# Kernel tuning notes

Hardware: AMD Instinct MI355X
Metric: run time of the kernel (lower is better)

Reference implementation:

```python
import jax, jax.numpy as jnp
import numpy as np

N_BANKS = 16
BAND = 4
D = 32          # n_neurons_per_hidd_bank
N_IN = 3072     # n_input_neurons
N_OUT = 1000    # n_output_neurons
B = 8192        # batch size
IDX_INPUT = [0, 1]
IDX_OUTPUT = [14, 15]
# edge list (source, target), target-major, ascending sources per target --
# matches the torch loop order (np.where over bank_conn[:, i_target])
EDGES = [(s, t) for t in range(N_BANKS) for s in range(max(0, t - BAND), t)]
E = len(EDGES)  # 54
TGT_EDGES = [[e for e, (s, t) in enumerate(EDGES) if t == tt] for tt in range(N_BANKS)]
BN_EPS = 1e-5


def _bn(a):
    # BatchNorm1d in training mode: batch mean, biased batch variance
    m = a.mean(axis=0)
    v = a.var(axis=0)
    return (a - m) * jax.lax.rsqrt(v + BN_EPS)


def setup_inputs() -> dict:
    key = jax.random.key(0)
    ks = jax.random.split(key, 8)
    return {
        "x": jax.random.normal(ks[0], (B, N_IN), jnp.float32),
        "bn_gamma": jnp.ones((N_IN,), jnp.float32),
        "bn_beta": jnp.zeros((N_IN,), jnp.float32),
        "W_in": jax.random.normal(ks[1], (len(IDX_INPUT), N_IN, D), jnp.float32) / np.float32(np.sqrt(N_IN)),
        "b_in": jax.random.normal(ks[2], (len(IDX_INPUT), D), jnp.float32) / np.float32(np.sqrt(N_IN)),
        "Wg": jax.random.normal(ks[3], (E, D), jnp.float32) / np.float32(np.sqrt(D)),
        "Wd": jax.random.normal(ks[4], (E, D, D), jnp.float32) / np.float32(np.sqrt(D)),
        "bd": jax.random.normal(ks[5], (E, D), jnp.float32) / np.float32(np.sqrt(D)),
        "Wout": jax.random.normal(ks[6], (len(IDX_OUTPUT), D, N_OUT), jnp.float32) / np.float32(np.sqrt(D)),
    }


def reference(x, bn_gamma, bn_beta, W_in, b_in, Wg, Wd, bd, Wout):
    # input batch norm (affine)
    x = _bn(x) * bn_gamma + bn_beta
    acts = [None] * N_BANKS
    for k, i in enumerate(IDX_INPUT):
        acts[i] = jax.nn.relu(x @ W_in[k] + b_in[k])  # [B, D]
    total_gate = jnp.zeros((x.shape[0], 1), x.dtype)
    for t in range(N_BANKS):
        acc = acts[t]  # non-None only for input banks
        for e in TGT_EDGES[t]:
            s = EDGES[e][0]
            gate = jnp.clip(acts[s] @ Wg[e], 0.0, 1.0)[:, None]  # hardtanh(.,0,1), [B,1]
            total_gate = total_gate + gate
            data = acts[s] @ Wd[e] + bd[e]                       # [B, D]
            acc = gate * data if acc is None else acc + gate * data
        acts[t] = _bn(jax.nn.relu(acc))  # hidden batch norm, affine=False
    output = None
    for k, i in enumerate(IDX_OUTPUT):
        d = acts[i] @ Wout[k]  # Linear(D, N_OUT, bias=False)
        output = d if output is None else output + d
    return output, total_gate
```

## Files before the change

kernel.cpp:

```cpp
#include <hip/hip_runtime.h>


#define BATCH 8192
#define NIN 3072
#define DD 32
#define NB 16
#define NOUT 1000
#define TGOFF (BATCH * NOUT)
#define BNEPS 1e-5f
#define NBLK 256
#define ROWS 32

#define O_SUM 0
#define O_FLAG 0
#define O_SUM2 3072
#define O_STATS2 6144
#define O_TG 22528
#define ZERO_FLOATS 30720
#define O_SCALE 30720
#define O_SHIFT 33792
#define O_BIAS 36864
#define O_BP 36928
#define O_ACTS 233536
#define O_ACC (O_ACTS + 2 * BATCH * DD)

__global__ void __launch_bounds__(256) k_stats(const float* __restrict__ x, float* __restrict__ ws) {
    int c = blockIdx.x * 256 + threadIdx.x;
    const float* p = x + (size_t)blockIdx.y * 128 * NIN + c;
    float s = 0.f, s2 = 0.f;
#pragma unroll 8
    for (int i = 0; i < 128; i++) { float v = p[(size_t)i * NIN]; s += v; s2 += v * v; }
    atomicAdd(&ws[O_SUM + c], s);
    atomicAdd(&ws[O_SUM2 + c], s2);
}

__global__ void __launch_bounds__(256) k_prep(float* __restrict__ ws, const float* __restrict__ g,
                                              const float* __restrict__ b, const float* __restrict__ b_in) {
    int c = blockIdx.x * 256 + threadIdx.x;
    float mean = ws[O_SUM + c] * (1.f / BATCH);
    float var = ws[O_SUM2 + c] * (1.f / BATCH) - mean * mean;
    float sc = g[c] * rsqrtf(fmaxf(var, 0.f) + BNEPS);
    ws[O_SCALE + c] = sc;
    ws[O_SHIFT + c] = b[c] - mean * sc;
    if (c < 64) ws[O_BIAS + c] = b_in[c];
}

__global__ void __launch_bounds__(256) k_bias(float* __restrict__ ws, const float* __restrict__ W_in) {
    int bank = blockIdx.x & 1, jc = blockIdx.x >> 1;
    int d = threadIdx.x & 31, js = threadIdx.x >> 5;
    int j0 = jc * 256 + js * 32;
    float a = 0.f;
    for (int j = 0; j < 32; j++)
        a += ws[O_SHIFT + j0 + j] * W_in[(size_t)bank * NIN * DD + (size_t)(j0 + j) * DD + d];
    __shared__ float red[8][32];
    red[js][d] = a;
    __syncthreads();
    if (threadIdx.x < 32) {
        float t = 0.f;
#pragma unroll
        for (int g8 = 0; g8 < 8; g8++) t += red[g8][threadIdx.x];
        atomicAdd(&ws[O_BIAS + bank * 32 + threadIdx.x], t);
    }
}

__global__ void __launch_bounds__(256) k_bfold(float* __restrict__ ws, const float* __restrict__ W_in) {
    int idx = blockIdx.x * 256 + threadIdx.x;
    int j = idx >> 6, c = idx & 63;
    ws[O_BP + idx] = ws[O_SCALE + j] * W_in[(size_t)(c >> 5) * NIN * DD + (size_t)j * DD + (c & 31)];
}

__global__ void __launch_bounds__(256) k_gemm3(const float* __restrict__ x, float* __restrict__ ws) {
    __shared__ float xL[64][20];
    __shared__ float bL[16][64];
    int tid = threadIdx.x;
    int row0 = blockIdx.x * 64;
    int k00 = blockIdx.y * 768;
    const float* bp = ws + O_BP;
    float acc[4][4] = {};
    int tx = tid & 15, rt = tid >> 4;
    int lr = tid >> 2, lq = tid & 3;
    int br = tid >> 4, bq = tid & 15;
    for (int kc = 0; kc < 48; kc++) {
        int k0 = k00 + kc * 16;
        float4 xv = *(const float4*)&x[(size_t)(row0 + lr) * NIN + k0 + lq * 4];
        float4 bv = *(const float4*)&bp[(size_t)(k0 + br) * 64 + bq * 4];
        __syncthreads();
        *(float4*)&xL[lr][lq * 4] = xv;
        *(float4*)&bL[br][bq * 4] = bv;
        __syncthreads();
#pragma unroll
        for (int kk = 0; kk < 16; kk += 4) {
            float4 b0 = *(float4*)&bL[kk][tx * 4];
            float4 b1 = *(float4*)&bL[kk + 1][tx * 4];
            float4 b2 = *(float4*)&bL[kk + 2][tx * 4];
            float4 b3 = *(float4*)&bL[kk + 3][tx * 4];
#pragma unroll
            for (int j = 0; j < 4; j++) {
                float4 xv4 = *(float4*)&xL[rt * 4 + j][kk];
                acc[j][0] += xv4.x * b0.x + xv4.y * b1.x + xv4.z * b2.x + xv4.w * b3.x;
                acc[j][1] += xv4.x * b0.y + xv4.y * b1.y + xv4.z * b2.y + xv4.w * b3.y;
                acc[j][2] += xv4.x * b0.z + xv4.y * b1.z + xv4.z * b2.z + xv4.w * b3.z;
                acc[j][3] += xv4.x * b0.w + xv4.y * b1.w + xv4.z * b2.w + xv4.w * b3.w;
            }
        }
    }
    float* dst = ws + O_ACC + (size_t)blockIdx.y * (BATCH * 64);
#pragma unroll
    for (int j = 0; j < 4; j++) {
        float4 v = make_float4(acc[j][0], acc[j][1], acc[j][2], acc[j][3]);
        *(float4*)&dst[(size_t)(row0 + rt * 4 + j) * 64 + tx * 4] = v;
    }
}

__global__ void __launch_bounds__(256) k_act(float* __restrict__ ws) {
    __shared__ float sred[16][32];
    __shared__ float qred[16][32];
    int tid = threadIdx.x;
    int i4 = (blockIdx.x * 256 + tid) * 4;
    const float* ac = ws + O_ACC;
    float4 s0 = *(const float4*)&ac[i4];
    float4 s1 = *(const float4*)&ac[524288 + i4];
    float4 s2 = *(const float4*)&ac[1048576 + i4];
    float4 s3 = *(const float4*)&ac[1572864 + i4];
    int c = i4 & 63, row = i4 >> 6;
    const float* bias = ws + O_BIAS;
    float4 v;
    v.x = fmaxf(s0.x + s1.x + s2.x + s3.x + bias[c], 0.f);
    v.y = fmaxf(s0.y + s1.y + s2.y + s3.y + bias[c + 1], 0.f);
    v.z = fmaxf(s0.z + s1.z + s2.z + s3.z + bias[c + 2], 0.f);
    v.w = fmaxf(s0.w + s1.w + s2.w + s3.w + bias[c + 3], 0.f);
    int bank = c >> 5, dd = c & 31;
    *(float4*)&ws[O_ACTS + ((size_t)bank * BATCH + row) * DD + dd] = v;
    int r16 = tid >> 4;
    if (bank == 0) {
        *(float4*)&sred[r16][dd] = v;
        *(float4*)&qred[r16][dd] = make_float4(v.x * v.x, v.y * v.y, v.z * v.z, v.w * v.w);
    }
    __syncthreads();
    if (tid < 32) {
        float sm = 0.f, sq = 0.f;
#pragma unroll
        for (int r = 0; r < 16; r++) { sm += sred[r][tid]; sq += qred[r][tid]; }
        int slot = blockIdx.x & 3;
        float* st = ws + O_STATS2 + (size_t)slot * 64;
        atomicAdd(&st[tid], sm);
        atomicAdd(&st[32 + tid], sq);
    }
}

__global__ void __launch_bounds__(256, 2) k_banks(float* __restrict__ ws,
                                                  const float* __restrict__ Wg,
                                                  const float* __restrict__ Wd,
                                                  const float* __restrict__ bd) {
    __shared__ float ring[4][ROWS][32];
    __shared__ float WdL[2][4][1024];
    __shared__ float sred4[4][64];
    __shared__ float m_s[32], iv_s[32];
    __shared__ float red[8][64];
    int tid = threadIdx.x;
    int rg = tid >> 5, d = tid & 31;
    int row0 = blockIdx.x * ROWS;
    int slot4 = blockIdx.x & 3;
    float* acts = ws + O_ACTS;
    float* stats = ws + O_STATS2;
    int* flag = (int*)(ws + O_FLAG);
    float tg[4] = {0.f, 0.f, 0.f, 0.f};
    float cur[4];
#pragma unroll
    for (int ri = 0; ri < 4; ri++) {
        int r = rg + 8 * ri;
        ring[0][r][d] = acts[(size_t)(row0 + r) * DD + d];
        cur[ri] = acts[((size_t)BATCH + row0 + r) * DD + d];
    }
    sred4[tid >> 6][tid & 63] = stats[(size_t)(tid >> 6) * 64 + (tid & 63)];
    __syncthreads();
    if (tid < 32) {
        float sm = sred4[0][tid] + sred4[1][tid] + sred4[2][tid] + sred4[3][tid];
        float sq = sred4[0][32 + tid] + sred4[1][32 + tid] + sred4[2][32 + tid] + sred4[3][32 + tid];
        float m = sm * (1.f / BATCH);
        float var = sq * (1.f / BATCH) - m * m;
        m_s[tid] = m;
        iv_s[tid] = rsqrtf(fmaxf(var, 0.f) + BNEPS);
    }
    ((float4*)&WdL[1][0][0])[tid] = ((const float4*)Wd)[tid];
    __syncthreads();
#pragma unroll
    for (int ri = 0; ri < 4; ri++) {
        int r = rg + 8 * ri;
        ring[0][r][d] = (ring[0][r][d] - m_s[d]) * iv_s[d];
    }
    __syncthreads();
    for (int t = 1; t < 16; t++) {
        int buf = t & 1;
        int nE = t < 4 ? t : 4;
        int s0 = t - nE;
        int eb = (t <= 4) ? t * (t - 1) / 2 : 10 + 4 * (t - 5);
        if (t < 15) {
            int t2 = t + 1;
            int nE2 = t2 < 4 ? t2 : 4;
            int eb2 = (t2 <= 4) ? t2 * (t2 - 1) / 2 : 10 + 4 * (t2 - 5);
            for (int p = tid; p < nE2 * 256; p += 256)
                ((float4*)&WdL[buf ^ 1][0][0])[p] = ((const float4*)(Wd + (size_t)eb2 * 1024))[p];
        }
        float wgr[4], bdr[4];
#pragma unroll
        for (int ei = 0; ei < 4; ei++) {
            wgr[ei] = (ei < nE) ? Wg[(eb + ei) * 32 + d] : 0.f;
            bdr[ei] = (ei < nE) ? bd[(eb + ei) * 32 + d] : 0.f;
        }
        float c_[4];
#pragma unroll
        for (int ri = 0; ri < 4; ri++) c_[ri] = (t == 1) ? cur[ri] : 0.f;
#pragma unroll
        for (int ei = 0; ei < 3; ei++) {
            if (ei < nE - 1) {
                int sl = (s0 + ei) & 3;
#pragma unroll
                for (int ri = 0; ri < 4; ri++) {
                    int r = rg + 8 * ri;
                    float g = ring[sl][r][d] * wgr[ei];
                    g += __shfl_xor(g, 1); g += __shfl_xor(g, 2); g += __shfl_xor(g, 4);
                    g += __shfl_xor(g, 8); g += __shfl_xor(g, 16);
                    g = fminf(fmaxf(g, 0.f), 1.f);
                    tg[ri] += g;
                    float dat = bdr[ei];
                    const float* ar = ring[sl][r];
                    const float* wc = &WdL[buf][ei][d];
#pragma unroll
                    for (int k = 0; k < 32; k += 4) {
                        float4 a4 = *(const float4*)&ar[k];
                        dat += a4.x * wc[k * 32] + a4.y * wc[(k + 1) * 32]
                             + a4.z * wc[(k + 2) * 32] + a4.w * wc[(k + 3) * 32];
                    }
                    c_[ri] += g * dat;
                }
            }
        }
        if (t > 1) {
            if (tid == 0) {
                while (__hip_atomic_load(&flag[t - 1], __ATOMIC_RELAXED, __HIP_MEMORY_SCOPE_AGENT) < NBLK)
                    __builtin_amdgcn_s_sleep(8);
            }
            __syncthreads();
            sred4[tid >> 6][tid & 63] = __hip_atomic_load(
                &stats[((size_t)(t - 1) * 4 + (tid >> 6)) * 64 + (tid & 63)],
                __ATOMIC_RELAXED, __HIP_MEMORY_SCOPE_AGENT);
            __syncthreads();
            if (tid < 32) {
                float sm = sred4[0][tid] + sred4[1][tid] + sred4[2][tid] + sred4[3][tid];
                float sq = sred4[0][32 + tid] + sred4[1][32 + tid] + sred4[2][32 + tid] + sred4[3][32 + tid];
                float m = sm * (1.f / BATCH);
                float var = sq * (1.f / BATCH) - m * m;
                m_s[tid] = m;
                iv_s[tid] = rsqrtf(fmaxf(var, 0.f) + BNEPS);
            }
            __syncthreads();
            int sl = (t - 1) & 3;
#pragma unroll
            for (int ri = 0; ri < 4; ri++) {
                int r = rg + 8 * ri;
                ring[sl][r][d] = (ring[sl][r][d] - m_s[d]) * iv_s[d];
            }
            __syncthreads();
        }
        {
            int ei = nE - 1;
            int sl = (t - 1) & 3;
#pragma unroll
            for (int ri = 0; ri < 4; ri++) {
                int r = rg + 8 * ri;
                float g = ring[sl][r][d] * wgr[ei];
                g += __shfl_xor(g, 1); g += __shfl_xor(g, 2); g += __shfl_xor(g, 4);
                g += __shfl_xor(g, 8); g += __shfl_xor(g, 16);
                g = fminf(fmaxf(g, 0.f), 1.f);
                tg[ri] += g;
                float dat = bdr[ei];
                const float* ar = ring[sl][r];
                const float* wc = &WdL[buf][ei][d];
#pragma unroll
                for (int k = 0; k < 32; k += 4) {
                    float4 a4 = *(const float4*)&ar[k];
                    dat += a4.x * wc[k * 32] + a4.y * wc[(k + 1) * 32]
                         + a4.z * wc[(k + 2) * 32] + a4.w * wc[(k + 3) * 32];
                }
                c_[ri] += g * dat;
            }
        }
        float vv[4];
#pragma unroll
        for (int ri = 0; ri < 4; ri++) vv[ri] = fmaxf(c_[ri], 0.f);
        __syncthreads();
#pragma unroll
        for (int ri = 0; ri < 4; ri++) {
            int r = rg + 8 * ri;
            ring[t & 3][r][d] = vv[ri];
            if (t >= 14) acts[((size_t)t * BATCH + row0 + r) * DD + d] = vv[ri];
        }
        red[rg][d] = vv[0] + vv[1] + vv[2] + vv[3];
        red[rg][32 + d] = vv[0] * vv[0] + vv[1] * vv[1] + vv[2] * vv[2] + vv[3] * vv[3];
        __syncthreads();
        if (tid < 64) {
            float a = 0.f;
#pragma unroll
            for (int g8 = 0; g8 < 8; g8++) a += red[g8][tid];
            atomicAdd(&stats[((size_t)t * 4 + slot4) * 64 + tid], a);
        }
        if (t < 15) {
            __syncthreads();
            if (tid == 0) atomicAdd(&flag[t], 1);
        }
    }
    if (d == 0) {
#pragma unroll
        for (int ri = 0; ri < 4; ri++) ws[O_TG + row0 + rg + 8 * ri] = tg[ri];
    }
}

__global__ void __launch_bounds__(256) k_out(const float* __restrict__ ws, const float* __restrict__ Wout,
                                             float* __restrict__ out) {
    __shared__ float aLt[32][68];
    __shared__ float wL[32][128];
    __shared__ float mIv[2][2][32];
    int tid = threadIdx.x;
    int row0 = blockIdx.x * 64;
    int col0 = blockIdx.y * 128;
    const float* acts = ws + O_ACTS;
    if (blockIdx.y == 0 && tid < 64) out[TGOFF + row0 + tid] = ws[O_TG + row0 + tid];
    if (tid < 64) {
        int bi = tid >> 5, d = tid & 31;
        const float* st = ws + O_STATS2 + (size_t)(14 + bi) * 4 * 64;
        float sm = 0.f, sq = 0.f;
#pragma unroll
        for (int sl = 0; sl < 4; sl++) { sm += st[sl * 64 + d]; sq += st[sl * 64 + 32 + d]; }
        float m = sm * (1.f / BATCH);
        float var = sq * (1.f / BATCH) - m * m;
        mIv[bi][0][d] = m;
        mIv[bi][1][d] = rsqrtf(fmaxf(var, 0.f) + BNEPS);
    }
    int tx = tid & 31, ty = tid >> 5;
    int c4 = col0 + tx * 4;
    bool c4ok = (c4 + 3 < NOUT);
    float acc[8][4] = {};
    for (int bi = 0; bi < 2; bi++) {
        __syncthreads();
        {
            int d = tid & 31, r0 = tid >> 5;
            float m = mIv[bi][0][d], iv = mIv[bi][1][d];
            const float* ap = acts + ((size_t)(14 + bi) * BATCH + row0) * DD + d;
#pragma unroll
            for (int i = 0; i < 8; i++) {
                int r = r0 + 8 * i;
                aLt[d][r] = (ap[(size_t)r * DD] - m) * iv;
            }
        }
        {
            const float* wp = Wout + (size_t)bi * DD * NOUT + c4;
            int kk0 = tid >> 5;
#pragma unroll
            for (int i = 0; i < 4; i++) {
                int kk = kk0 + 8 * i;
                const float* wr = wp + (size_t)kk * NOUT;
                float4 v;
                if (c4ok) {
                    v = *(const float4*)wr;
                } else {
                    v.x = (c4 + 0 < NOUT) ? wr[0] : 0.f;
                    v.y = (c4 + 1 < NOUT) ? wr[1] : 0.f;
                    v.z = (c4 + 2 < NOUT) ? wr[2] : 0.f;
                    v.w = (c4 + 3 < NOUT) ? wr[3] : 0.f;
                }
                *(float4*)&wL[kk][tx * 4] = v;
            }
        }
        __syncthreads();
#pragma unroll 4
        for (int k = 0; k < 32; k++) {
            float4 w = *(float4*)&wL[k][tx * 4];
            float4 a0 = *(float4*)&aLt[k][ty * 8];
            float4 a1 = *(float4*)&aLt[k][ty * 8 + 4];
            float ar[8] = {a0.x, a0.y, a0.z, a0.w, a1.x, a1.y, a1.z, a1.w};
            float wc[4] = {w.x, w.y, w.z, w.w};
#pragma unroll
            for (int r = 0; r < 8; r++)
#pragma unroll
                for (int c = 0; c < 4; c++)
                    acc[r][c] += ar[r] * wc[c];
        }
    }
    if (c4ok) {
#pragma unroll
        for (int r = 0; r < 8; r++) {
            int row = row0 + ty * 8 + r;
            *(float4*)&out[(size_t)row * NOUT + c4] =
                make_float4(acc[r][0], acc[r][1], acc[r][2], acc[r][3]);
        }
    } else {
#pragma unroll
        for (int r = 0; r < 8; r++) {
            int row = row0 + ty * 8 + r;
#pragma unroll
            for (int c = 0; c < 4; c++)
                if (c4 + c < NOUT) out[(size_t)row * NOUT + c4 + c] = acc[r][c];
        }
    }
}

extern "C" void kernel_launch(void* const* d_in, const int* in_sizes, int n_in,
                              void* d_out, int out_size, void* d_ws, size_t ws_size,
                              hipStream_t stream) {
    (void)in_sizes; (void)n_in; (void)out_size; (void)ws_size;
    const float* x     = (const float*)d_in[0];
    const float* gamma = (const float*)d_in[1];
    const float* beta  = (const float*)d_in[2];
    const float* W_in  = (const float*)d_in[3];
    const float* b_in  = (const float*)d_in[4];
    const float* Wg    = (const float*)d_in[5];
    const float* Wd    = (const float*)d_in[6];
    const float* bd    = (const float*)d_in[7];
    const float* Wout  = (const float*)d_in[8];
    float* out = (float*)d_out;
    float* ws  = (float*)d_ws;

    hipMemsetAsync(d_ws, 0, ZERO_FLOATS * sizeof(float), stream);
    k_stats<<<dim3(12, 64), 256, 0, stream>>>(x, ws);
    k_prep<<<12, 256, 0, stream>>>(ws, gamma, beta, b_in);
    k_bias<<<24, 256, 0, stream>>>(ws, W_in);
    k_bfold<<<768, 256, 0, stream>>>(ws, W_in);
    k_gemm3<<<dim3(128, 4), 256, 0, stream>>>(x, ws);
    k_act<<<512, 256, 0, stream>>>(ws);
    hipMemsetAsync(ws + O_FLAG, 0, 16 * sizeof(int), stream);
    k_banks<<<NBLK, 256, 0, stream>>>(ws, Wg, Wd, bd);
    k_out<<<dim3(128, 8), 256, 0, stream>>>(ws, Wout, out);
}
```

Baseline: 375.8 us.

## Split input GEMM finer and spread bank-sync stats and flags over eight slots

The input-projection GEMM now uses 32-row tiles with 6-way split-K, launching 1536 blocks instead of 512 so more CUs stay busy. k_act sums six partial slices to match. In the bank pipeline, batch-norm statistics and completion flags are spread over 8 slots instead of 4 and a single counter, to cut atomic contention. Waiting blocks poll the eight flag counters with one wavefront and sleep for shorter intervals. The cost is more split-K partial traffic and a larger workspace for the partial sums.

```diff
diff --git a/kernel.cpp b/kernel.cpp
--- a/kernel.cpp
+++ b/kernel.cpp
@@ -10,6 +10,7 @@
 #define BNEPS 1e-5f
 #define NBLK 256
 #define ROWS 32
+#define NSLOT 8
 
 #define O_SUM 0
 #define O_FLAG 0
@@ -70,22 +71,22 @@
 }
 
 __global__ void __launch_bounds__(256) k_gemm3(const float* __restrict__ x, float* __restrict__ ws) {
-    __shared__ float xL[64][20];
+    __shared__ float xL[32][20];
     __shared__ float bL[16][64];
     int tid = threadIdx.x;
-    int row0 = blockIdx.x * 64;
-    int k00 = blockIdx.y * 768;
+    int row0 = blockIdx.x * 32;
+    int k00 = blockIdx.y * 512;
     const float* bp = ws + O_BP;
-    float acc[4][4] = {};
+    float acc[2][4] = {};
     int tx = tid & 15, rt = tid >> 4;
-    int lr = tid >> 2, lq = tid & 3;
+    int lr = tid >> 3, lq = tid & 7;
     int br = tid >> 4, bq = tid & 15;
-    for (int kc = 0; kc < 48; kc++) {
+    for (int kc = 0; kc < 32; kc++) {
         int k0 = k00 + kc * 16;
-        float4 xv = *(const float4*)&x[(size_t)(row0 + lr) * NIN + k0 + lq * 4];
+        float2 xv = *(const float2*)&x[(size_t)(row0 + lr) * NIN + k0 + lq * 2];
         float4 bv = *(const float4*)&bp[(size_t)(k0 + br) * 64 + bq * 4];
         __syncthreads();
-        *(float4*)&xL[lr][lq * 4] = xv;
+        *(float2*)&xL[lr][lq * 2] = xv;
         *(float4*)&bL[br][bq * 4] = bv;
         __syncthreads();
 #pragma unroll
@@ -95,8 +96,8 @@
             float4 b2 = *(float4*)&bL[kk + 2][tx * 4];
             float4 b3 = *(float4*)&bL[kk + 3][tx * 4];
 #pragma unroll
-            for (int j = 0; j < 4; j++) {
-                float4 xv4 = *(float4*)&xL[rt * 4 + j][kk];
+            for (int j = 0; j < 2; j++) {
+                float4 xv4 = *(float4*)&xL[rt * 2 + j][kk];
                 acc[j][0] += xv4.x * b0.x + xv4.y * b1.x + xv4.z * b2.x + xv4.w * b3.x;
                 acc[j][1] += xv4.x * b0.y + xv4.y * b1.y + xv4.z * b2.y + xv4.w * b3.y;
                 acc[j][2] += xv4.x * b0.z + xv4.y * b1.z + xv4.z * b2.z + xv4.w * b3.z;
@@ -106,9 +107,9 @@
     }
     float* dst = ws + O_ACC + (size_t)blockIdx.y * (BATCH * 64);
 #pragma unroll
-    for (int j = 0; j < 4; j++) {
+    for (int j = 0; j < 2; j++) {
         float4 v = make_float4(acc[j][0], acc[j][1], acc[j][2], acc[j][3]);
-        *(float4*)&dst[(size_t)(row0 + rt * 4 + j) * 64 + tx * 4] = v;
+        *(float4*)&dst[(size_t)(row0 + rt * 2 + j) * 64 + tx * 4] = v;
     }
 }
 
@@ -122,13 +123,15 @@
     float4 s1 = *(const float4*)&ac[524288 + i4];
     float4 s2 = *(const float4*)&ac[1048576 + i4];
     float4 s3 = *(const float4*)&ac[1572864 + i4];
+    float4 s4 = *(const float4*)&ac[2097152 + i4];
+    float4 s5 = *(const float4*)&ac[2621440 + i4];
     int c = i4 & 63, row = i4 >> 6;
     const float* bias = ws + O_BIAS;
     float4 v;
-    v.x = fmaxf(s0.x + s1.x + s2.x + s3.x + bias[c], 0.f);
-    v.y = fmaxf(s0.y + s1.y + s2.y + s3.y + bias[c + 1], 0.f);
-    v.z = fmaxf(s0.z + s1.z + s2.z + s3.z + bias[c + 2], 0.f);
-    v.w = fmaxf(s0.w + s1.w + s2.w + s3.w + bias[c + 3], 0.f);
+    v.x = fmaxf(s0.x + s1.x + s2.x + s3.x + s4.x + s5.x + bias[c], 0.f);
+    v.y = fmaxf(s0.y + s1.y + s2.y + s3.y + s4.y + s5.y + bias[c + 1], 0.f);
+    v.z = fmaxf(s0.z + s1.z + s2.z + s3.z + s4.z + s5.z + bias[c + 2], 0.f);
+    v.w = fmaxf(s0.w + s1.w + s2.w + s3.w + s4.w + s5.w + bias[c + 3], 0.f);
     int bank = c >> 5, dd = c & 31;
     *(float4*)&ws[O_ACTS + ((size_t)bank * BATCH + row) * DD + dd] = v;
     int r16 = tid >> 4;
@@ -141,7 +144,7 @@
         float sm = 0.f, sq = 0.f;
 #pragma unroll
         for (int r = 0; r < 16; r++) { sm += sred[r][tid]; sq += qred[r][tid]; }
-        int slot = blockIdx.x & 3;
+        int slot = blockIdx.x & (NSLOT - 1);
         float* st = ws + O_STATS2 + (size_t)slot * 64;
         atomicAdd(&st[tid], sm);
         atomicAdd(&st[32 + tid], sq);
@@ -154,13 +157,13 @@
                                                   const float* __restrict__ bd) {
     __shared__ float ring[4][ROWS][32];
     __shared__ float WdL[2][4][1024];
-    __shared__ float sred4[4][64];
+    __shared__ float sred8[512];
     __shared__ float m_s[32], iv_s[32];
     __shared__ float red[8][64];
     int tid = threadIdx.x;
     int rg = tid >> 5, d = tid & 31;
     int row0 = blockIdx.x * ROWS;
-    int slot4 = blockIdx.x & 3;
+    int slot8 = blockIdx.x & (NSLOT - 1);
     float* acts = ws + O_ACTS;
     float* stats = ws + O_STATS2;
     int* flag = (int*)(ws + O_FLAG);
@@ -172,11 +175,13 @@
         ring[0][r][d] = acts[(size_t)(row0 + r) * DD + d];
         cur[ri] = acts[((size_t)BATCH + row0 + r) * DD + d];
     }
-    sred4[tid >> 6][tid & 63] = stats[(size_t)(tid >> 6) * 64 + (tid & 63)];
+    sred8[tid] = stats[tid];
+    sred8[tid + 256] = stats[tid + 256];
     __syncthreads();
     if (tid < 32) {
-        float sm = sred4[0][tid] + sred4[1][tid] + sred4[2][tid] + sred4[3][tid];
-        float sq = sred4[0][32 + tid] + sred4[1][32 + tid] + sred4[2][32 + tid] + sred4[3][32 + tid];
+        float sm = 0.f, sq = 0.f;
+#pragma unroll
+        for (int s = 0; s < NSLOT; s++) { sm += sred8[s * 64 + tid]; sq += sred8[s * 64 + 32 + tid]; }
         float m = sm * (1.f / BATCH);
         float var = sq * (1.f / BATCH) - m * m;
         m_s[tid] = m;
@@ -237,18 +242,28 @@
             }
         }
         if (t > 1) {
-            if (tid == 0) {
-                while (__hip_atomic_load(&flag[t - 1], __ATOMIC_RELAXED, __HIP_MEMORY_SCOPE_AGENT) < NBLK)
-                    __builtin_amdgcn_s_sleep(8);
+            if (tid < 64) {
+                int done = 0;
+                while (!done) {
+                    int f = (tid < NSLOT)
+                        ? __hip_atomic_load(&flag[(t - 1) * NSLOT + tid], __ATOMIC_RELAXED, __HIP_MEMORY_SCOPE_AGENT)
+                        : 0;
+                    f += __shfl_xor(f, 1); f += __shfl_xor(f, 2); f += __shfl_xor(f, 4);
+                    done = (__shfl(f, 0) >= NBLK);
+                    if (!done) __builtin_amdgcn_s_sleep(2);
+                }
             }
             __syncthreads();
-            sred4[tid >> 6][tid & 63] = __hip_atomic_load(
-                &stats[((size_t)(t - 1) * 4 + (tid >> 6)) * 64 + (tid & 63)],
-                __ATOMIC_RELAXED, __HIP_MEMORY_SCOPE_AGENT);
+            {
+                const float* st = stats + (size_t)(t - 1) * NSLOT * 64;
+                sred8[tid] = __hip_atomic_load(&st[tid], __ATOMIC_RELAXED, __HIP_MEMORY_SCOPE_AGENT);
+                sred8[tid + 256] = __hip_atomic_load(&st[tid + 256], __ATOMIC_RELAXED, __HIP_MEMORY_SCOPE_AGENT);
+            }
             __syncthreads();
             if (tid < 32) {
-                float sm = sred4[0][tid] + sred4[1][tid] + sred4[2][tid] + sred4[3][tid];
-                float sq = sred4[0][32 + tid] + sred4[1][32 + tid] + sred4[2][32 + tid] + sred4[3][32 + tid];
+                float sm = 0.f, sq = 0.f;
+#pragma unroll
+                for (int s = 0; s < NSLOT; s++) { sm += sred8[s * 64 + tid]; sq += sred8[s * 64 + 32 + tid]; }
                 float m = sm * (1.f / BATCH);
                 float var = sq * (1.f / BATCH) - m * m;
                 m_s[tid] = m;
@@ -303,11 +318,11 @@
             float a = 0.f;
 #pragma unroll
             for (int g8 = 0; g8 < 8; g8++) a += red[g8][tid];
-            atomicAdd(&stats[((size_t)t * 4 + slot4) * 64 + tid], a);
+            atomicAdd(&stats[((size_t)t * NSLOT + slot8) * 64 + tid], a);
         }
         if (t < 15) {
             __syncthreads();
-            if (tid == 0) atomicAdd(&flag[t], 1);
+            if (tid == 0) atomicAdd(&flag[t * NSLOT + slot8], 1);
         }
     }
     if (d == 0) {
@@ -328,10 +343,10 @@
     if (blockIdx.y == 0 && tid < 64) out[TGOFF + row0 + tid] = ws[O_TG + row0 + tid];
     if (tid < 64) {
         int bi = tid >> 5, d = tid & 31;
-        const float* st = ws + O_STATS2 + (size_t)(14 + bi) * 4 * 64;
+        const float* st = ws + O_STATS2 + (size_t)(14 + bi) * NSLOT * 64;
         float sm = 0.f, sq = 0.f;
 #pragma unroll
-        for (int sl = 0; sl < 4; sl++) { sm += st[sl * 64 + d]; sq += st[sl * 64 + 32 + d]; }
+        for (int sl = 0; sl < NSLOT; sl++) { sm += st[sl * 64 + d]; sq += st[sl * 64 + 32 + d]; }
         float m = sm * (1.f / BATCH);
         float var = sq * (1.f / BATCH) - m * m;
         mIv[bi][0][d] = m;
@@ -426,9 +441,9 @@
     k_prep<<<12, 256, 0, stream>>>(ws, gamma, beta, b_in);
     k_bias<<<24, 256, 0, stream>>>(ws, W_in);
     k_bfold<<<768, 256, 0, stream>>>(ws, W_in);
-    k_gemm3<<<dim3(128, 4), 256, 0, stream>>>(x, ws);
+    k_gemm3<<<dim3(256, 6), 256, 0, stream>>>(x, ws);
     k_act<<<512, 256, 0, stream>>>(ws);
-    hipMemsetAsync(ws + O_FLAG, 0, 16 * sizeof(int), stream);
+    hipMemsetAsync(ws + O_FLAG, 0, NB * NSLOT * sizeof(int), stream);
     k_banks<<<NBLK, 256, 0, stream>>>(ws, Wg, Wd, bd);
     k_out<<<dim3(128, 8), 256, 0, stream>>>(ws, Wout, out);
 }
```

Measured after the change: 377.6 us. No clear change (+0.5%).
